# Optimization experiments

Hardware: AMD Instinct MI355X
Metric: run time of the kernel (lower is better)

## Reference

```python
import jax, jax.numpy as jnp
import numpy as np

B = 1024          # batch
S = 2048          # sparseDim == obsDim (required by PhiW shape constraints)
FISTA_ITER = 16


def setup_inputs() -> dict:
    key = jax.random.key(0)
    k1, k2, k3 = jax.random.split(key, 3)
    src = jax.random.normal(k1, (B, S, 1), dtype=jnp.float32)
    Y = jax.random.normal(k2, (B, S, 1), dtype=jnp.float32)
    W = jax.random.normal(k3, (S, S), dtype=jnp.float32)
    # F.normalize(W, p=2, dim=0): unit L2 norm per column
    W = W / jnp.linalg.norm(W, axis=0, keepdims=True)
    alpha = jnp.full((1, 1), 0.1, dtype=jnp.float32)  # alpha_initialize
    return {"src": src, "Y": Y, "W": W, "alpha": alpha}


def reference(src, Y, W, alpha):
    obsDim = W.shape[0]          # == sparseDim == S
    # Lipschitz constant: max |eig(W^T W)|; W^T W is symmetric PSD so eigvalsh is exact
    L = jnp.max(jnp.linalg.eigvalsh(W.T @ W))
    thresh = alpha / L * 0.5     # soft-threshold level, shape [1,1]

    def phiW(x):
        theta_m = x[:, :obsDim]          # [B, S, 1]
        delta = x[:, obsDim:]            # [B, S, 1]
        return src * jnp.matmul(W, theta_m) + delta

    def phiWT(y):
        return jnp.concatenate((jnp.matmul(W.T, src * y), y), axis=1)  # [B, 2S, 1]

    nb = Y.shape[0]
    x0 = jnp.zeros((nb, 2 * obsDim, 1), dtype=Y.dtype)

    def step(carry, _):
        x_old, y_k, t_old = carry
        res = Y - phiW(y_k)
        v = y_k + phiWT(res) / L
        x_new = jnp.sign(v) * jnp.maximum(jnp.abs(v) - thresh, 0.0)
        t_new = (1.0 + jnp.sqrt(1.0 + 4.0 * t_old * t_old)) / 2.0
        y_new = x_new + (t_old - 1.0) / t_new * (x_new - x_old)
        return (x_new, y_new, t_new), None

    (x_new, _, _), _ = jax.lax.scan(
        step, (x0, x0, jnp.float32(1.0)), None, length=FISTA_ITER
    )
    return x_new
```

## Files before the change

### kernel.cpp

```cpp
#include <hip/hip_runtime.h>
#include <math.h>

#define SDIM 2048
#define BATCH 1024
#define NITER 16
#define LM 40

typedef unsigned short ushort_t;
typedef __attribute__((ext_vector_type(8))) short bf16x8;
typedef __attribute__((ext_vector_type(4))) float f32x4;

#define MFMA(a,b,c) __builtin_amdgcn_mfma_f32_16x16x32_bf16((a),(b),(c),0,0,0)

__device__ __forceinline__ float softt(float v, float th){
  return copysignf(fmaxf(fabsf(v) - th, 0.0f), v);
}

__device__ __forceinline__ float bf2f(ushort_t h){
  return __uint_as_float(((unsigned)h) << 16);
}

__device__ __forceinline__ void split2(float x, ushort_t* h, ushort_t* l){
  unsigned u = __float_as_uint(x);
  unsigned hh = (u + 0x7FFFu + ((u >> 16) & 1u)) >> 16;
  float hf = __uint_as_float(hh << 16);
  float r = x - hf;
  unsigned v = __float_as_uint(r);
  unsigned ll = (v + 0x7FFFu + ((v >> 16) & 1u)) >> 16;
  *h = (ushort_t)hh; *l = (ushort_t)ll;
}

__device__ __forceinline__ void cp16(const ushort_t* g, ushort_t* l){
  __builtin_amdgcn_global_load_lds(
      (const __attribute__((address_space(1))) unsigned int*)g,
      (__attribute__((address_space(3))) unsigned int*)l, 16, 0, 0);
}

__device__ __forceinline__ void gemm_core(ushort_t* __restrict__ sm,
                                          const ushort_t* __restrict__ Ah, const ushort_t* __restrict__ Al,
                                          const ushort_t* __restrict__ Bh, const ushort_t* __restrict__ Bl,
                                          int m0, int n0, int K, f32x4 acc[2][2])
{
  ushort_t* lAh = sm;
  ushort_t* lAl = sm + 4096;
  ushort_t* lBh = sm + 8192;
  ushort_t* lBl = sm + 12288;
  const int tid = threadIdx.x;
  const int rr = tid >> 3;
  const int kp = (tid & 7) ^ (rr & 7);
  const size_t strA = (size_t)32 * K;
  const ushort_t* gAh = Ah + (size_t)(m0 + rr) * K + kp * 8;
  const ushort_t* gAl = Al + (size_t)(m0 + rr) * K + kp * 8;
  const ushort_t* gBh = Bh + (size_t)(n0 + rr) * K + kp * 8;
  const ushort_t* gBl = Bl + (size_t)(n0 + rr) * K + kp * 8;
  ushort_t* dA0 = &lAh[tid * 8];      ushort_t* dA1 = &lAh[(tid + 256) * 8];
  ushort_t* dAl0 = &lAl[tid * 8];     ushort_t* dAl1 = &lAl[(tid + 256) * 8];
  ushort_t* dB0 = &lBh[tid * 8];      ushort_t* dB1 = &lBh[(tid + 256) * 8];
  ushort_t* dBl0 = &lBl[tid * 8];     ushort_t* dBl1 = &lBl[(tid + 256) * 8];

  const int lane = tid & 63, wv = tid >> 6;
  const int wm = (wv >> 1) * 32, wn = (wv & 1) * 32;
  const int mm = lane & 15, quad = lane >> 4;
  const int ra0 = wm + mm, ra1 = wm + 16 + mm;
  const int rb0 = wn + mm, rb1 = wn + 16 + mm;
  int oa0[2], oa1[2], ob0[2], ob1[2];
  #pragma unroll
  for (int u = 0; u < 2; u++){
    oa0[u] = ra0*64 + (((u*4 + quad) ^ (ra0 & 7)) << 3);
    oa1[u] = ra1*64 + (((u*4 + quad) ^ (ra1 & 7)) << 3);
    ob0[u] = rb0*64 + (((u*4 + quad) ^ (rb0 & 7)) << 3);
    ob1[u] = rb1*64 + (((u*4 + quad) ^ (rb1 & 7)) << 3);
  }

  const int nk = K / 64;
  cp16(gAh, dA0); cp16(gAh + strA, dA1);
  cp16(gAl, dAl0); cp16(gAl + strA, dAl1);
  cp16(gBh, dB0); cp16(gBh + strA, dB1);
  cp16(gBl, dBl0); cp16(gBl + strA, dBl1);
  gAh += 64; gAl += 64; gBh += 64; gBl += 64;

  for (int kt = 0; kt < nk; kt++){
    __syncthreads();
    bf16x8 ah0[2], ah1[2], al0[2], al1[2], bh0[2], bh1[2], bl0[2], bl1[2];
    #pragma unroll
    for (int u = 0; u < 2; u++){
      ah0[u] = *(const bf16x8*)&lAh[oa0[u]];
      ah1[u] = *(const bf16x8*)&lAh[oa1[u]];
      al0[u] = *(const bf16x8*)&lAl[oa0[u]];
      al1[u] = *(const bf16x8*)&lAl[oa1[u]];
      bh0[u] = *(const bf16x8*)&lBh[ob0[u]];
      bh1[u] = *(const bf16x8*)&lBh[ob1[u]];
      bl0[u] = *(const bf16x8*)&lBl[ob0[u]];
      bl1[u] = *(const bf16x8*)&lBl[ob1[u]];
    }
    __syncthreads();
    if (kt + 1 < nk){
      cp16(gAh, dA0); cp16(gAh + strA, dA1);
      cp16(gAl, dAl0); cp16(gAl + strA, dAl1);
      cp16(gBh, dB0); cp16(gBh + strA, dB1);
      cp16(gBl, dBl0); cp16(gBl + strA, dBl1);
      gAh += 64; gAl += 64; gBh += 64; gBl += 64;
    }
    #pragma unroll
    for (int u = 0; u < 2; u++){
      acc[0][0] = MFMA(ah0[u], bh0[u], acc[0][0]);
      acc[0][0] = MFMA(ah0[u], bl0[u], acc[0][0]);
      acc[0][0] = MFMA(al0[u], bh0[u], acc[0][0]);
      acc[0][1] = MFMA(ah0[u], bh1[u], acc[0][1]);
      acc[0][1] = MFMA(ah0[u], bl1[u], acc[0][1]);
      acc[0][1] = MFMA(al0[u], bh1[u], acc[0][1]);
      acc[1][0] = MFMA(ah1[u], bh0[u], acc[1][0]);
      acc[1][0] = MFMA(ah1[u], bl0[u], acc[1][0]);
      acc[1][0] = MFMA(al1[u], bh0[u], acc[1][0]);
      acc[1][1] = MFMA(ah1[u], bh1[u], acc[1][1]);
      acc[1][1] = MFMA(ah1[u], bl1[u], acc[1][1]);
      acc[1][1] = MFMA(al1[u], bh1[u], acc[1][1]);
    }
  }
}

__device__ __forceinline__ void acc_to_tile(ushort_t* sm, f32x4 acc[2][2]){
  float* tile = (float*)sm;
  const int tid = threadIdx.x, lane = tid & 63, wv = tid >> 6;
  const int wm = (wv >> 1) * 32, wn = (wv & 1) * 32;
  const int mm = lane & 15, quad = lane >> 4;
  #pragma unroll
  for (int tm = 0; tm < 2; tm++)
    #pragma unroll
    for (int tn = 0; tn < 2; tn++)
      #pragma unroll
      for (int i = 0; i < 4; i++)
        tile[(wm + tm*16 + quad*4 + i)*65 + wn + tn*16 + mm] = acc[tm][tn][i];
  __syncthreads();
}

#define EPILOGUE_FOR(rowvar, c4var) \
  const int tid = threadIdx.x, lane = tid & 63, wv = tid >> 6; \
  const int r4 = lane >> 4; \
  const int c4var = (lane & 15) * 4; \
  for (int j = 0; j < 4; j++){ \
    const int rowvar = wv*16 + j*4 + r4;

__global__ __launch_bounds__(256) void k_split(const float* __restrict__ W,
                                               ushort_t* __restrict__ Wah, ushort_t* __restrict__ Wal,
                                               ushort_t* __restrict__ Wbh, ushort_t* __restrict__ Wbl){
  __shared__ float t[32][33];
  const int i0 = blockIdx.y * 32, j0 = blockIdx.x * 32;
  const int r = threadIdx.x >> 3, c = (threadIdx.x & 7) * 4;
  const float4 v = *(const float4*)&W[(size_t)(i0 + r) * SDIM + j0 + c];
  float vv[4] = {v.x, v.y, v.z, v.w};
  ushort_t h[4], l[4];
  #pragma unroll
  for (int q = 0; q < 4; q++){ split2(vv[q], &h[q], &l[q]); t[r][c+q] = vv[q]; }
  *(ushort4*)&Wah[(size_t)(i0 + r) * SDIM + j0 + c] = make_ushort4(h[0],h[1],h[2],h[3]);
  *(ushort4*)&Wal[(size_t)(i0 + r) * SDIM + j0 + c] = make_ushort4(l[0],l[1],l[2],l[3]);
  __syncthreads();
  #pragma unroll
  for (int q = 0; q < 4; q++) split2(t[c+q][r], &h[q], &l[q]);
  *(ushort4*)&Wbh[(size_t)(j0 + r) * SDIM + i0 + c] = make_ushort4(h[0],h[1],h[2],h[3]);
  *(ushort4*)&Wbl[(size_t)(j0 + r) * SDIM + i0 + c] = make_ushort4(l[0],l[1],l[2],l[3]);
}

__global__ __launch_bounds__(256) void k_gemmM(const ushort_t* __restrict__ Wah, const ushort_t* __restrict__ Wal,
                                               float* __restrict__ Mmat){
  __shared__ __align__(16) ushort_t smem[16384];
  const int b = blockIdx.x + (blockIdx.y << 5);
  const int xcd = b & 7, slot = b >> 3;
  const int n0 = (((xcd << 2) + (slot >> 5)) << 6);
  const int m0 = ((slot & 31) << 6);
  f32x4 acc[2][2] = {};
  gemm_core(smem, Wah, Wal, Wah, Wal, m0, n0, SDIM, acc);
  acc_to_tile(smem, acc);
  const float* tile = (const float*)smem;
  EPILOGUE_FOR(row, c4)
    f32x4 a = *(const f32x4*)&tile[row*65 + c4];
    *(f32x4*)&Mmat[(size_t)(m0 + row) * SDIM + n0 + c4] = a;
  }
}

__global__ __launch_bounds__(256) void k_init(float* __restrict__ vRing,
                                              double* __restrict__ dotWV, double* __restrict__ dotWW,
                                              float* __restrict__ betaSq){
  __shared__ float red[256];
  int t = threadIdx.x;
  float vals[8];
  float s = 0.f;
  #pragma unroll
  for (int p = 0; p < 8; p++){
    int j = p*256 + t;
    unsigned h = (unsigned)j * 2654435761u;
    h ^= h >> 16; h *= 2246822519u; h ^= h >> 13;
    float r = (float)(h & 0xFFFFFFu) / 16777216.0f - 0.5f;
    vals[p] = r; s += r*r;
  }
  red[t] = s; __syncthreads();
  for (int o = 128; o > 0; o >>= 1){ if (t < o) red[t] += red[t+o]; __syncthreads(); }
  float inv = rsqrtf(red[0]);
  #pragma unroll
  for (int p = 0; p < 8; p++){
    int j = p*256 + t;
    vRing[SDIM + j] = vals[p]*inv;
    vRing[j] = 0.f;
    vRing[2*SDIM + j] = 0.f;
  }
  if (t < LM+2){ dotWV[t] = 0.0; dotWW[t] = 0.0; betaSq[t] = 0.f; }
}

__global__ __launch_bounds__(256) void k_lstep(const float* __restrict__ M,
    const float* __restrict__ wOld, float* __restrict__ wNew,
    float* __restrict__ vRing, double* __restrict__ dotWV, double* __restrict__ dotWW,
    float* __restrict__ betaSq, int s){
  __shared__ float vs[SDIM];
  __shared__ double pAl[4], pWw[4];
  const int tid = threadIdx.x, bid = blockIdx.x;
  if (s == 1){
    const float* v1 = vRing + SDIM;
    for (int j = tid; j < SDIM; j += 256) vs[j] = v1[j];
  } else {
    const double a  = dotWV[s-1];
    const double ww = dotWW[s-1];
    const float bpSq = betaSq[s-2];
    float bsq = (float)(ww - a*a - (double)bpSq);
    bsq = fmaxf(bsq, 1e-20f);
    const float beta = sqrtf(bsq), invb = 1.0f/beta;
    const float alpha = (float)a, bprev = sqrtf(bpSq);
    const float* vm1 = vRing + ((s-1)%3)*SDIM;
    const float* vm2 = vRing + ((s-2)%3)*SDIM;
    float* vdst = vRing + (s%3)*SDIM;
    for (int j = tid; j < SDIM; j += 256){
      float val = (wOld[j] - alpha*vm1[j] - bprev*vm2[j]) * invb;
      vs[j] = val;
      if (bid == 0) vdst[j] = val;
    }
    if (bid == 0 && tid == 0) betaSq[s-1] = bsq;
  }
  __syncthreads();
  const int wv = tid >> 6, lane = tid & 63;
  const int row = bid*4 + wv;
  const float4* Mr = (const float4*)(M + (size_t)row * SDIM);
  const float4* v4 = (const float4*)vs;
  float acc = 0.f;
  #pragma unroll
  for (int p = 0; p < 8; p++){
    int j4 = p*64 + lane;
    float4 m = Mr[j4], v = v4[j4];
    acc += m.x*v.x + m.y*v.y + m.z*v.z + m.w*v.w;
  }
  #pragma unroll
  for (int o = 32; o > 0; o >>= 1) acc += __shfl_down(acc, o);
  if (lane == 0){
    wNew[row] = acc;
    pAl[wv] = (double)acc * (double)vs[row];
    pWw[wv] = (double)acc * (double)acc;
  }
  __syncthreads();
  if (tid == 0){
    atomicAdd(&dotWV[s], pAl[0]+pAl[1]+pAl[2]+pAl[3]);
    atomicAdd(&dotWW[s], pWw[0]+pWw[1]+pWw[2]+pWw[3]);
  }
}

__global__ void k_sturm(const double* __restrict__ dotWV, const float* __restrict__ betaSq,
                        const float* __restrict__ alphaIn, float* __restrict__ Lbuf){
  __shared__ double sa[LM+1], sb[LM+1];
  int lane = threadIdx.x;
  for (int i = lane; i <= LM; i += 64){
    if (i >= 1){
      sa[i] = dotWV[i];
      sb[i] = (i < LM) ? sqrt((double)betaSq[i]) : 0.0;
    }
  }
  __syncthreads();
  double phi = -1e300, plo = 1e300;
  for (int i = 1 + lane; i <= LM; i += 64){
    double r = (i > 1 ? sb[i-1] : 0.0) + (i < LM ? sb[i] : 0.0);
    phi = fmax(phi, sa[i] + r);
    plo = fmin(plo, sa[i] - r);
  }
  for (int o = 32; o > 0; o >>= 1){
    phi = fmax(phi, __shfl_down(phi, o));
    plo = fmin(plo, __shfl_down(plo, o));
  }
  double hi = __shfl(phi, 0), lo = __shfl(plo, 0);
  for (int round = 0; round < 6; round++){
    double x = lo + (hi - lo) * (double)(lane + 1) / 65.0;
    int cnt = 0;
    double dd = sa[1] - x;
    if (dd < 0) cnt++;
    for (int i = 2; i <= LM; i++){
      double off = sb[i-1];
      if (fabs(dd) < 1e-300) dd = -1e-300;
      dd = sa[i] - x - off*off/dd;
      if (dd < 0) cnt++;
    }
    unsigned long long bal = __ballot(cnt == LM);
    int p = (bal == 0ull) ? 64 : (__ffsll((unsigned long long)bal) - 1);
    double newhi = (p <= 63) ? lo + (hi - lo) * (double)(p + 1) / 65.0 : hi;
    double newlo = (p >= 1)  ? lo + (hi - lo) * (double)p / 65.0       : lo;
    hi = newhi; lo = newlo;
  }
  if (lane == 0){
    double L = 0.5*(lo + hi);
    Lbuf[0] = (float)(1.0 / L);
    Lbuf[1] = (float)(0.5 * (double)alphaIn[0] / L);
  }
}


__global__ __launch_bounds__(256) void k_A0(const float* __restrict__ Y, const float* __restrict__ src,
                                            float* __restrict__ yd, ushort_t* __restrict__ sresh,
                                            ushort_t* __restrict__ sresl, float* __restrict__ out,
                                            const float* __restrict__ Lbuf){
  int idx = blockIdx.x*256 + threadIdx.x;
  float invL = Lbuf[0], th = Lbuf[1];
  float y = Y[idx], s = src[idx];
  split2(s*y, &sresh[idx], &sresl[idx]);
  float xn = softt(y*invL, th);
  int b = idx >> 11, i = idx & 2047;
  out[(size_t)b*4096 + 2048 + i] = xn;
  yd[idx] = xn;
}

__device__ __forceinline__ void swz512(int* m0, int* n0){
  const int b = blockIdx.x + (blockIdx.y << 5);
  const int xcd = b & 7, slot = b >> 3;
  *n0 = (((xcd << 2) + (slot >> 4)) << 6);
  *m0 = ((slot & 15) << 6);
}

__global__ __launch_bounds__(256) void k_gemmA(
    const ushort_t* __restrict__ Wah, const ushort_t* __restrict__ Wal,
    const ushort_t* __restrict__ ymh, const ushort_t* __restrict__ yml,
    const float* __restrict__ Y, const float* __restrict__ src,
    float* __restrict__ yd, float* __restrict__ out,
    ushort_t* __restrict__ sresh, ushort_t* __restrict__ sresl,
    const float* __restrict__ Lbuf, float ck)
{
  __shared__ __align__(16) ushort_t smem[16384];
  f32x4 acc[2][2] = {};
  int m0, n0; swz512(&m0, &n0);
  gemm_core(smem, ymh, yml, Wah, Wal, m0, n0, SDIM, acc);
  acc_to_tile(smem, acc);
  const float* tile = (const float*)smem;
  const float invL = Lbuf[0], th = Lbuf[1];
  EPILOGUE_FOR(row, c4)
    const int brow = m0 + row;
    const size_t g  = (size_t)brow*SDIM + n0 + c4;
    const size_t go = (size_t)brow*4096 + 2048 + n0 + c4;
    f32x4 a   = *(const f32x4*)&tile[row*65 + c4];
    f32x4 s4  = *(const f32x4*)&src[g];
    f32x4 y4  = *(const f32x4*)&Y[g];
    f32x4 yd4 = *(const f32x4*)&yd[g];
    f32x4 xo4 = *(const f32x4*)&out[go];
    f32x4 res, xn, yn;
    ushort4 sh, sl;
    #pragma unroll
    for (int q = 0; q < 4; q++){
      res[q] = y4[q] - s4[q]*a[q] - yd4[q];
      xn[q]  = softt(yd4[q] + res[q]*invL, th);
      yn[q]  = xn[q] + ck*(xn[q] - xo4[q]);
    }
    split2(s4[0]*res[0], &sh.x, &sl.x);
    split2(s4[1]*res[1], &sh.y, &sl.y);
    split2(s4[2]*res[2], &sh.z, &sl.z);
    split2(s4[3]*res[3], &sh.w, &sl.w);
    *(ushort4*)&sresh[g] = sh;
    *(ushort4*)&sresl[g] = sl;
    *(f32x4*)&out[go] = xn;
    *(f32x4*)&yd[g]   = yn;
  }
}

template<bool FIRST>
__global__ __launch_bounds__(256) void k_gemmB(
    const ushort_t* __restrict__ Wbh, const ushort_t* __restrict__ Wbl,
    const ushort_t* __restrict__ sresh, const ushort_t* __restrict__ sresl,
    ushort_t* __restrict__ ymh, ushort_t* __restrict__ yml,
    float* __restrict__ out, const float* __restrict__ Lbuf, float ck)
{
  __shared__ __align__(16) ushort_t smem[16384];
  f32x4 acc[2][2] = {};
  int m0, n0; swz512(&m0, &n0);
  gemm_core(smem, sresh, sresl, Wbh, Wbl, m0, n0, SDIM, acc);
  acc_to_tile(smem, acc);
  const float* tile = (const float*)smem;
  const float invL = Lbuf[0], th = Lbuf[1];
  EPILOGUE_FOR(row, c4)
    const int brow = m0 + row;
    const size_t g  = (size_t)brow*SDIM + n0 + c4;
    const size_t go = (size_t)brow*4096 + n0 + c4;
    f32x4 a = *(const f32x4*)&tile[row*65 + c4];
    f32x4 ym4, xo4;
    if (FIRST){
      ym4 = (f32x4){0.f,0.f,0.f,0.f};
      xo4 = (f32x4){0.f,0.f,0.f,0.f};
    } else {
      ushort4 h4 = *(const ushort4*)&ymh[g];
      ushort4 l4 = *(const ushort4*)&yml[g];
      ym4[0] = bf2f(h4.x) + bf2f(l4.x);
      ym4[1] = bf2f(h4.y) + bf2f(l4.y);
      ym4[2] = bf2f(h4.z) + bf2f(l4.z);
      ym4[3] = bf2f(h4.w) + bf2f(l4.w);
      xo4 = *(const f32x4*)&out[go];
    }
    f32x4 xn, yn;
    ushort4 hh, ll;
    #pragma unroll
    for (int q = 0; q < 4; q++){
      xn[q] = softt(ym4[q] + a[q]*invL, th);
      yn[q] = xn[q] + ck*(xn[q] - xo4[q]);
    }
    split2(yn[0], &hh.x, &ll.x);
    split2(yn[1], &hh.y, &ll.y);
    split2(yn[2], &hh.z, &ll.z);
    split2(yn[3], &hh.w, &ll.w);
    *(f32x4*)&out[go] = xn;
    *(ushort4*)&ymh[g] = hh;
    *(ushort4*)&yml[g] = ll;
  }
}


extern "C" void kernel_launch(void* const* d_in, const int* in_sizes, int n_in,
                              void* d_out, int out_size, void* d_ws, size_t ws_size,
                              hipStream_t stream) {
  const float* src   = (const float*)d_in[0];
  const float* Y     = (const float*)d_in[1];
  const float* W     = (const float*)d_in[2];
  const float* alpha = (const float*)d_in[3];
  float* out = (float*)d_out;
  float* ws  = (float*)d_ws;

  const size_t M1 = 1024*1024;
  float* Mmat = ws;
  float* yd   = ws + 4*M1;
  float* lanc = ws + 6*M1;
  float* w0      = lanc;
  float* w1      = lanc + SDIM;
  float* vRing   = lanc + 2*SDIM;
  double* dotWV  = (double*)(lanc + 5*SDIM);
  double* dotWW  = dotWV + 128;
  float* betaSq  = lanc + 5*SDIM + 512;
  float* Lbuf    = betaSq + 128;
  ushort_t* u16 = (ushort_t*)(ws + 7*M1);
  ushort_t* Wah = u16;
  ushort_t* Wal = u16 + 4*M1;
  ushort_t* Wbh = u16 + 8*M1;
  ushort_t* Wbl = u16 + 12*M1;
  ushort_t* ymh = u16 + 16*M1;
  ushort_t* yml = u16 + 18*M1;
  ushort_t* sresh = u16 + 20*M1;
  ushort_t* sresl = u16 + 22*M1;

  k_split<<<dim3(64,64), 256, 0, stream>>>(W, Wah, Wal, Wbh, Wbl);
  k_gemmM<<<dim3(32,32), 256, 0, stream>>>(Wah, Wal, Mmat);

  float* wb[2] = { w0, w1 };
  k_init<<<1, 256, 0, stream>>>(vRing, dotWV, dotWW, betaSq);
  for (int s = 1; s <= LM; s++){
    k_lstep<<<512, 256, 0, stream>>>(Mmat, wb[(s+1)&1], wb[s&1], vRing, dotWV, dotWW, betaSq, s);
  }
  k_sturm<<<1, 64, 0, stream>>>(dotWV, betaSq, alpha, Lbuf);

  double t = 1.0;
  float ckv[NITER];
  for (int k = 0; k < NITER; k++){
    double tn = 0.5*(1.0 + sqrt(1.0 + 4.0*t*t));
    ckv[k] = (float)((t - 1.0)/tn);
    t = tn;
  }

  k_A0<<<(BATCH*SDIM)/256, 256, 0, stream>>>(Y, src, yd, sresh, sresl, out, Lbuf);
  k_gemmB<true><<<dim3(32,16), 256, 0, stream>>>(Wbh, Wbl, sresh, sresl, ymh, yml, out, Lbuf, ckv[0]);
  for (int k = 1; k < NITER; k++){
    k_gemmA<<<dim3(32,16), 256, 0, stream>>>(Wah, Wal, ymh, yml, Y, src, yd, out, sresh, sresl, Lbuf, ckv[k]);
    k_gemmB<false><<<dim3(32,16), 256, 0, stream>>>(Wbh, Wbl, sresh, sresl, ymh, yml, out, Lbuf, ckv[k]);
  }
  (void)in_sizes; (void)n_in; (void)out_size; (void)ws_size;
}
```

Measured before the change: 1.708 ms.

## Pre-pack W into MFMA fragment layout and load B operand directly to registers

The split kernel now writes the bf16 hi/lo copies of W and W^T in a 16x32 fragment-tiled layout that matches the MFMA operand layout. The GEMM core then reads the W operand straight from global memory into registers, double-buffered one k-step ahead, instead of staging it through LDS. Only the activation operand still goes through LDS, which halves LDS usage and the LDS read traffic per step. The trade-off is that W tiles are no longer shared through LDS across waves, so each wave issues its own global loads, and there is more register pressure from the prefetched fragments.

```diff
diff --git a/kernel.cpp b/kernel.cpp
--- a/kernel.cpp
+++ b/kernel.cpp
@@ -36,87 +36,128 @@
       (__attribute__((address_space(3))) unsigned int*)l, 16, 0, 0);
 }
 
-__device__ __forceinline__ void gemm_core(ushort_t* __restrict__ sm,
-                                          const ushort_t* __restrict__ Ah, const ushort_t* __restrict__ Al,
-                                          const ushort_t* __restrict__ Bh, const ushort_t* __restrict__ Bl,
-                                          int m0, int n0, int K, f32x4 acc[2][2])
+template<bool AFRAG>
+__device__ __forceinline__ void gemm_core3(ushort_t* __restrict__ sm,
+    const ushort_t* __restrict__ Ah, const ushort_t* __restrict__ Al,
+    const ushort_t* __restrict__ Bfh, const ushort_t* __restrict__ Bfl,
+    int m0, int n0, int K, f32x4 acc[2][2])
 {
-  ushort_t* lAh = sm;
-  ushort_t* lAl = sm + 4096;
-  ushort_t* lBh = sm + 8192;
-  ushort_t* lBl = sm + 12288;
   const int tid = threadIdx.x;
-  const int rr = tid >> 3;
-  const int kp = (tid & 7) ^ (rr & 7);
-  const size_t strA = (size_t)32 * K;
-  const ushort_t* gAh = Ah + (size_t)(m0 + rr) * K + kp * 8;
-  const ushort_t* gAl = Al + (size_t)(m0 + rr) * K + kp * 8;
-  const ushort_t* gBh = Bh + (size_t)(n0 + rr) * K + kp * 8;
-  const ushort_t* gBl = Bl + (size_t)(n0 + rr) * K + kp * 8;
-  ushort_t* dA0 = &lAh[tid * 8];      ushort_t* dA1 = &lAh[(tid + 256) * 8];
-  ushort_t* dAl0 = &lAl[tid * 8];     ushort_t* dAl1 = &lAl[(tid + 256) * 8];
-  ushort_t* dB0 = &lBh[tid * 8];      ushort_t* dB1 = &lBh[(tid + 256) * 8];
-  ushort_t* dBl0 = &lBl[tid * 8];     ushort_t* dBl1 = &lBl[(tid + 256) * 8];
-
   const int lane = tid & 63, wv = tid >> 6;
-  const int wm = (wv >> 1) * 32, wn = (wv & 1) * 32;
+  const int wm = (wv >> 1) * 32;
   const int mm = lane & 15, quad = lane >> 4;
-  const int ra0 = wm + mm, ra1 = wm + 16 + mm;
-  const int rb0 = wn + mm, rb1 = wn + 16 + mm;
-  int oa0[2], oa1[2], ob0[2], ob1[2];
-  #pragma unroll
-  for (int u = 0; u < 2; u++){
-    oa0[u] = ra0*64 + (((u*4 + quad) ^ (ra0 & 7)) << 3);
-    oa1[u] = ra1*64 + (((u*4 + quad) ^ (ra1 & 7)) << 3);
-    ob0[u] = rb0*64 + (((u*4 + quad) ^ (rb0 & 7)) << 3);
-    ob1[u] = rb1*64 + (((u*4 + quad) ^ (rb1 & 7)) << 3);
-  }
-
-  const int nk = K / 64;
-  cp16(gAh, dA0); cp16(gAh + strA, dA1);
-  cp16(gAl, dAl0); cp16(gAl + strA, dAl1);
-  cp16(gBh, dB0); cp16(gBh + strA, dB1);
-  cp16(gBl, dBl0); cp16(gBl + strA, dBl1);
-  gAh += 64; gAl += 64; gBh += 64; gBl += 64;
-
-  for (int kt = 0; kt < nk; kt++){
-    __syncthreads();
-    bf16x8 ah0[2], ah1[2], al0[2], al1[2], bh0[2], bh1[2], bl0[2], bl1[2];
+  const int KS = K >> 5;
+
+  const ushort_t *gA0, *gA1, *gA2, *gA3;
+  int astep;
+  if (!AFRAG){
+    const int rr = tid >> 3;
+    const int kp = (tid & 7) ^ (rr & 7);
+    gA0 = Ah + (size_t)(m0 + rr) * K + kp * 8;
+    gA1 = Ah + (size_t)(m0 + rr + 32) * K + kp * 8;
+    gA2 = Al + (size_t)(m0 + rr) * K + kp * 8;
+    gA3 = Al + (size_t)(m0 + rr + 32) * K + kp * 8;
+    astep = 64;
+  } else {
+    const int nt0 = m0 >> 4;
+    const int id0 = tid, id1 = tid + 256;
+    gA0 = Ah + ((size_t)(nt0 + (id0 >> 7)) * KS + ((id0 >> 6) & 1)) * 512 + (id0 & 63) * 8;
+    gA1 = Ah + ((size_t)(nt0 + (id1 >> 7)) * KS + ((id1 >> 6) & 1)) * 512 + (id1 & 63) * 8;
+    gA2 = Al + ((size_t)(nt0 + (id0 >> 7)) * KS + ((id0 >> 6) & 1)) * 512 + (id0 & 63) * 8;
+    gA3 = Al + ((size_t)(nt0 + (id1 >> 7)) * KS + ((id1 >> 6) & 1)) * 512 + (id1 & 63) * 8;
+    astep = 1024;
+  }
+  ushort_t* dA0 = &sm[tid * 8];
+  ushort_t* dA1 = &sm[(tid + 256) * 8];
+  ushort_t* dA2 = &sm[4096 + tid * 8];
+  ushort_t* dA3 = &sm[4096 + (tid + 256) * 8];
+
+  int oa[2][2];
+  if (!AFRAG){
+    #pragma unroll
+    for (int s = 0; s < 2; s++){
+      const int ra = wm + s*16 + mm;
+      #pragma unroll
+      for (int u = 0; u < 2; u++)
+        oa[s][u] = ra*64 + (((u*4 + quad) ^ (ra & 7)) << 3);
+    }
+  } else {
+    #pragma unroll
+    for (int s = 0; s < 2; s++){
+      const int ntl = (wv >> 1)*2 + s;
+      #pragma unroll
+      for (int u = 0; u < 2; u++)
+        oa[s][u] = (ntl*2 + u)*512 + lane*8;
+    }
+  }
+
+  const ushort_t* pBh[2]; const ushort_t* pBl[2];
+  #pragma unroll
+  for (int s = 0; s < 2; s++){
+    const int nt = (n0 >> 4) + (wv & 1)*2 + s;
+    pBh[s] = Bfh + (size_t)nt * KS * 512 + lane*8;
+    pBl[s] = Bfl + (size_t)nt * KS * 512 + lane*8;
+  }
+
+  const int nk = K >> 6;
+  cp16(gA0, dA0); cp16(gA1, dA1); cp16(gA2, dA2); cp16(gA3, dA3);
+  bf16x8 bhP[2][2], blP[2][2], bhQ[2][2], blQ[2][2];
+  #pragma unroll
+  for (int s = 0; s < 2; s++)
     #pragma unroll
     for (int u = 0; u < 2; u++){
-      ah0[u] = *(const bf16x8*)&lAh[oa0[u]];
-      ah1[u] = *(const bf16x8*)&lAh[oa1[u]];
-      al0[u] = *(const bf16x8*)&lAl[oa0[u]];
-      al1[u] = *(const bf16x8*)&lAl[oa1[u]];
-      bh0[u] = *(const bf16x8*)&lBh[ob0[u]];
-      bh1[u] = *(const bf16x8*)&lBh[ob1[u]];
-      bl0[u] = *(const bf16x8*)&lBl[ob0[u]];
-      bl1[u] = *(const bf16x8*)&lBl[ob1[u]];
-    }
-    __syncthreads();
-    if (kt + 1 < nk){
-      cp16(gAh, dA0); cp16(gAh + strA, dA1);
-      cp16(gAl, dAl0); cp16(gAl + strA, dAl1);
-      cp16(gBh, dB0); cp16(gBh + strA, dB1);
-      cp16(gBl, dBl0); cp16(gBl + strA, dBl1);
-      gAh += 64; gAl += 64; gBh += 64; gBl += 64;
-    }
-    #pragma unroll
-    for (int u = 0; u < 2; u++){
-      acc[0][0] = MFMA(ah0[u], bh0[u], acc[0][0]);
-      acc[0][0] = MFMA(ah0[u], bl0[u], acc[0][0]);
-      acc[0][0] = MFMA(al0[u], bh0[u], acc[0][0]);
-      acc[0][1] = MFMA(ah0[u], bh1[u], acc[0][1]);
-      acc[0][1] = MFMA(ah0[u], bl1[u], acc[0][1]);
-      acc[0][1] = MFMA(al0[u], bh1[u], acc[0][1]);
-      acc[1][0] = MFMA(ah1[u], bh0[u], acc[1][0]);
-      acc[1][0] = MFMA(ah1[u], bl0[u], acc[1][0]);
-      acc[1][0] = MFMA(al1[u], bh0[u], acc[1][0]);
-      acc[1][1] = MFMA(ah1[u], bh1[u], acc[1][1]);
-      acc[1][1] = MFMA(ah1[u], bl1[u], acc[1][1]);
-      acc[1][1] = MFMA(al1[u], bh1[u], acc[1][1]);
-    }
-  }
+      bhP[s][u] = *(const bf16x8*)(pBh[s] + (size_t)u*512);
+      blP[s][u] = *(const bf16x8*)(pBl[s] + (size_t)u*512);
+    }
+
+#define GK_STEP(KT, BH, BL, BHN, BLN, PF) { \
+    __syncthreads();   \
+    bf16x8 ah[2][2], al8[2][2]; \
+    _Pragma("unroll") \
+    for (int s = 0; s < 2; s++){ \
+      _Pragma("unroll") \
+      for (int u = 0; u < 2; u++){ \
+        ah[s][u]  = *(const bf16x8*)&sm[oa[s][u]]; \
+        al8[s][u] = *(const bf16x8*)&sm[4096 + oa[s][u]]; \
+      } \
+    } \
+    __syncthreads();   \
+    if (PF){ \
+      const size_t ao = (size_t)(KT + 1) * astep; \
+      cp16(gA0 + ao, dA0); cp16(gA1 + ao, dA1); \
+      cp16(gA2 + ao, dA2); cp16(gA3 + ao, dA3); \
+      const size_t bo = (size_t)(KT + 1) * 1024; \
+      _Pragma("unroll") \
+      for (int s = 0; s < 2; s++){ \
+        _Pragma("unroll") \
+        for (int u = 0; u < 2; u++){ \
+          BHN[s][u] = *(const bf16x8*)(pBh[s] + bo + u*512); \
+          BLN[s][u] = *(const bf16x8*)(pBl[s] + bo + u*512); \
+        } \
+      } \
+    } \
+    _Pragma("unroll") \
+    for (int u = 0; u < 2; u++){ \
+      acc[0][0] = MFMA(ah[0][u],  BH[0][u], acc[0][0]); \
+      acc[0][0] = MFMA(ah[0][u],  BL[0][u], acc[0][0]); \
+      acc[0][0] = MFMA(al8[0][u], BH[0][u], acc[0][0]); \
+      acc[0][1] = MFMA(ah[0][u],  BH[1][u], acc[0][1]); \
+      acc[0][1] = MFMA(ah[0][u],  BL[1][u], acc[0][1]); \
+      acc[0][1] = MFMA(al8[0][u], BH[1][u], acc[0][1]); \
+      acc[1][0] = MFMA(ah[1][u],  BH[0][u], acc[1][0]); \
+      acc[1][0] = MFMA(ah[1][u],  BL[0][u], acc[1][0]); \
+      acc[1][0] = MFMA(al8[1][u], BH[0][u], acc[1][0]); \
+      acc[1][1] = MFMA(ah[1][u],  BH[1][u], acc[1][1]); \
+      acc[1][1] = MFMA(ah[1][u],  BL[1][u], acc[1][1]); \
+      acc[1][1] = MFMA(al8[1][u], BH[1][u], acc[1][1]); \
+    } \
+  }
+
+  for (int kt = 0; kt < nk; kt += 2){
+    GK_STEP(kt,     bhP, blP, bhQ, blQ, true);
+    GK_STEP(kt + 1, bhQ, blQ, bhP, blP, (kt + 2 < nk));
+  }
+#undef GK_STEP
 }
 
 __device__ __forceinline__ void acc_to_tile(ushort_t* sm, f32x4 acc[2][2]){
@@ -142,8 +183,8 @@
     const int rowvar = wv*16 + j*4 + r4;
 
 __global__ __launch_bounds__(256) void k_split(const float* __restrict__ W,
-                                               ushort_t* __restrict__ Wah, ushort_t* __restrict__ Wal,
-                                               ushort_t* __restrict__ Wbh, ushort_t* __restrict__ Wbl){
+        ushort_t* __restrict__ Wfa_h, ushort_t* __restrict__ Wfa_l,
+        ushort_t* __restrict__ Wfb_h, ushort_t* __restrict__ Wfb_l){
   __shared__ float t[32][33];
   const int i0 = blockIdx.y * 32, j0 = blockIdx.x * 32;
   const int r = threadIdx.x >> 3, c = (threadIdx.x & 7) * 4;
@@ -152,24 +193,35 @@
   ushort_t h[4], l[4];
   #pragma unroll
   for (int q = 0; q < 4; q++){ split2(vv[q], &h[q], &l[q]); t[r][c+q] = vv[q]; }
-  *(ushort4*)&Wah[(size_t)(i0 + r) * SDIM + j0 + c] = make_ushort4(h[0],h[1],h[2],h[3]);
-  *(ushort4*)&Wal[(size_t)(i0 + r) * SDIM + j0 + c] = make_ushort4(l[0],l[1],l[2],l[3]);
+  {
+    const int row = i0 + r, col = j0 + c;
+    const size_t idx = ((size_t)(row >> 4) * 64 + (col >> 5)) * 512
+                     + (size_t)((col >> 3) & 3) * 128 + (row & 15) * 8 + (col & 7);
+    *(ushort4*)&Wfa_h[idx] = make_ushort4(h[0],h[1],h[2],h[3]);
+    *(ushort4*)&Wfa_l[idx] = make_ushort4(l[0],l[1],l[2],l[3]);
+  }
   __syncthreads();
   #pragma unroll
   for (int q = 0; q < 4; q++) split2(t[c+q][r], &h[q], &l[q]);
-  *(ushort4*)&Wbh[(size_t)(j0 + r) * SDIM + i0 + c] = make_ushort4(h[0],h[1],h[2],h[3]);
-  *(ushort4*)&Wbl[(size_t)(j0 + r) * SDIM + i0 + c] = make_ushort4(l[0],l[1],l[2],l[3]);
-}
-
-__global__ __launch_bounds__(256) void k_gemmM(const ushort_t* __restrict__ Wah, const ushort_t* __restrict__ Wal,
+  {
+    const int row = j0 + r, col = i0 + c;
+    const size_t idx = ((size_t)(row >> 4) * 64 + (col >> 5)) * 512
+                     + (size_t)((col >> 3) & 3) * 128 + (row & 15) * 8 + (col & 7);
+    *(ushort4*)&Wfb_h[idx] = make_ushort4(h[0],h[1],h[2],h[3]);
+    *(ushort4*)&Wfb_l[idx] = make_ushort4(l[0],l[1],l[2],l[3]);
+  }
+}
+
+__global__ __launch_bounds__(256) void k_gemmM(const ushort_t* __restrict__ Wfa_h,
+                                               const ushort_t* __restrict__ Wfa_l,
                                                float* __restrict__ Mmat){
-  __shared__ __align__(16) ushort_t smem[16384];
+  __shared__ __align__(16) ushort_t smem[8320];
   const int b = blockIdx.x + (blockIdx.y << 5);
   const int xcd = b & 7, slot = b >> 3;
   const int n0 = (((xcd << 2) + (slot >> 5)) << 6);
   const int m0 = ((slot & 31) << 6);
   f32x4 acc[2][2] = {};
-  gemm_core(smem, Wah, Wal, Wah, Wal, m0, n0, SDIM, acc);
+  gemm_core3<true>(smem, Wfa_h, Wfa_l, Wfa_h, Wfa_l, m0, n0, SDIM, acc);
   acc_to_tile(smem, acc);
   const float* tile = (const float*)smem;
   EPILOGUE_FOR(row, c4)
@@ -329,17 +381,17 @@
 }
 
 __global__ __launch_bounds__(256) void k_gemmA(
-    const ushort_t* __restrict__ Wah, const ushort_t* __restrict__ Wal,
+    const ushort_t* __restrict__ Wfa_h, const ushort_t* __restrict__ Wfa_l,
     const ushort_t* __restrict__ ymh, const ushort_t* __restrict__ yml,
     const float* __restrict__ Y, const float* __restrict__ src,
     float* __restrict__ yd, float* __restrict__ out,
     ushort_t* __restrict__ sresh, ushort_t* __restrict__ sresl,
     const float* __restrict__ Lbuf, float ck)
 {
-  __shared__ __align__(16) ushort_t smem[16384];
+  __shared__ __align__(16) ushort_t smem[8320];
   f32x4 acc[2][2] = {};
   int m0, n0; swz512(&m0, &n0);
-  gemm_core(smem, ymh, yml, Wah, Wal, m0, n0, SDIM, acc);
+  gemm_core3<false>(smem, ymh, yml, Wfa_h, Wfa_l, m0, n0, SDIM, acc);
   acc_to_tile(smem, acc);
   const float* tile = (const float*)smem;
   const float invL = Lbuf[0], th = Lbuf[1];
@@ -373,15 +425,15 @@
 
 template<bool FIRST>
 __global__ __launch_bounds__(256) void k_gemmB(
-    const ushort_t* __restrict__ Wbh, const ushort_t* __restrict__ Wbl,
+    const ushort_t* __restrict__ Wfb_h, const ushort_t* __restrict__ Wfb_l,
     const ushort_t* __restrict__ sresh, const ushort_t* __restrict__ sresl,
     ushort_t* __restrict__ ymh, ushort_t* __restrict__ yml,
     float* __restrict__ out, const float* __restrict__ Lbuf, float ck)
 {
-  __shared__ __align__(16) ushort_t smem[16384];
+  __shared__ __align__(16) ushort_t smem[8320];
   f32x4 acc[2][2] = {};
   int m0, n0; swz512(&m0, &n0);
-  gemm_core(smem, sresh, sresl, Wbh, Wbl, m0, n0, SDIM, acc);
+  gemm_core3<false>(smem, sresh, sresl, Wfb_h, Wfb_l, m0, n0, SDIM, acc);
   acc_to_tile(smem, acc);
   const float* tile = (const float*)smem;
   const float invL = Lbuf[0], th = Lbuf[1];
@@ -443,17 +495,17 @@
   float* betaSq  = lanc + 5*SDIM + 512;
   float* Lbuf    = betaSq + 128;
   ushort_t* u16 = (ushort_t*)(ws + 7*M1);
-  ushort_t* Wah = u16;
-  ushort_t* Wal = u16 + 4*M1;
-  ushort_t* Wbh = u16 + 8*M1;
-  ushort_t* Wbl = u16 + 12*M1;
+  ushort_t* Wfa_h = u16;
+  ushort_t* Wfa_l = u16 + 4*M1;
+  ushort_t* Wfb_h = u16 + 8*M1;
+  ushort_t* Wfb_l = u16 + 12*M1;
   ushort_t* ymh = u16 + 16*M1;
   ushort_t* yml = u16 + 18*M1;
   ushort_t* sresh = u16 + 20*M1;
   ushort_t* sresl = u16 + 22*M1;
 
-  k_split<<<dim3(64,64), 256, 0, stream>>>(W, Wah, Wal, Wbh, Wbl);
-  k_gemmM<<<dim3(32,32), 256, 0, stream>>>(Wah, Wal, Mmat);
+  k_split<<<dim3(64,64), 256, 0, stream>>>(W, Wfa_h, Wfa_l, Wfb_h, Wfb_l);
+  k_gemmM<<<dim3(32,32), 256, 0, stream>>>(Wfa_h, Wfa_l, Mmat);
 
   float* wb[2] = { w0, w1 };
   k_init<<<1, 256, 0, stream>>>(vRing, dotWV, dotWW, betaSq);
@@ -471,10 +523,10 @@
   }
 
   k_A0<<<(BATCH*SDIM)/256, 256, 0, stream>>>(Y, src, yd, sresh, sresl, out, Lbuf);
-  k_gemmB<true><<<dim3(32,16), 256, 0, stream>>>(Wbh, Wbl, sresh, sresl, ymh, yml, out, Lbuf, ckv[0]);
+  k_gemmB<true><<<dim3(32,16), 256, 0, stream>>>(Wfb_h, Wfb_l, sresh, sresl, ymh, yml, out, Lbuf, ckv[0]);
   for (int k = 1; k < NITER; k++){
-    k_gemmA<<<dim3(32,16), 256, 0, stream>>>(Wah, Wal, ymh, yml, Y, src, yd, out, sresh, sresl, Lbuf, ckv[k]);
-    k_gemmB<false><<<dim3(32,16), 256, 0, stream>>>(Wbh, Wbl, sresh, sresl, ymh, yml, out, Lbuf, ckv[k]);
+    k_gemmA<<<dim3(32,16), 256, 0, stream>>>(Wfa_h, Wfa_l, ymh, yml, Y, src, yd, out, sresh, sresl, Lbuf, ckv[k]);
+    k_gemmB<false><<<dim3(32,16), 256, 0, stream>>>(Wfb_h, Wfb_l, sresh, sresl, ymh, yml, out, Lbuf, ckv[k]);
   }
   (void)in_sizes; (void)n_in; (void)out_size; (void)ws_size;
 }
```

Measured after the change: 1.969 ms. 1.15x slower.

## Use triple-buffered K=32 LDS pipeline with vmcnt waits in GEMM core

Applied to the files above, without the earlier changes.

Replaces the single-buffer K=64 GEMM mainloop with a three-stage ring of K=32 tiles. Global-to-LDS loads run two stages ahead, and each iteration uses one s_waitcnt vmcnt plus a barrier instead of two __syncthreads. MFMA issue is wrapped in s_setprio to favour the math waves. This is meant to hide global load latency and cut barrier stalls, at the cost of more LDS per block (48KB), which could lower occupancy, and more loop iterations.

```diff
diff --git a/kernel.cpp b/kernel.cpp
--- a/kernel.cpp
+++ b/kernel.cpp
@@ -36,90 +36,79 @@
       (__attribute__((address_space(3))) unsigned int*)l, 16, 0, 0);
 }
 
-__device__ __forceinline__ void gemm_core(ushort_t* __restrict__ sm,
-                                          const ushort_t* __restrict__ Ah, const ushort_t* __restrict__ Al,
-                                          const ushort_t* __restrict__ Bh, const ushort_t* __restrict__ Bl,
-                                          int m0, int n0, int K, f32x4 acc[2][2])
+__device__ __forceinline__ void gemm_core5(ushort_t* __restrict__ sm,
+    const ushort_t* __restrict__ Ah, const ushort_t* __restrict__ Al,
+    const ushort_t* __restrict__ Bh, const ushort_t* __restrict__ Bl,
+    int m0, int n0, int K, f32x4 acc[2][2])
 {
-  ushort_t* lAh = sm;
-  ushort_t* lAl = sm + 4096;
-  ushort_t* lBh = sm + 8192;
-  ushort_t* lBl = sm + 12288;
   const int tid = threadIdx.x;
-  const int rr = tid >> 3;
-  const int kp = (tid & 7) ^ (rr & 7);
-  const size_t strA = (size_t)32 * K;
+  const int rr = tid >> 2;
+  const int kc = tid & 3;
+  const int kp = kc ^ (rr & 3);
   const ushort_t* gAh = Ah + (size_t)(m0 + rr) * K + kp * 8;
   const ushort_t* gAl = Al + (size_t)(m0 + rr) * K + kp * 8;
   const ushort_t* gBh = Bh + (size_t)(n0 + rr) * K + kp * 8;
   const ushort_t* gBl = Bl + (size_t)(n0 + rr) * K + kp * 8;
-  ushort_t* dA0 = &lAh[tid * 8];      ushort_t* dA1 = &lAh[(tid + 256) * 8];
-  ushort_t* dAl0 = &lAl[tid * 8];     ushort_t* dAl1 = &lAl[(tid + 256) * 8];
-  ushort_t* dB0 = &lBh[tid * 8];      ushort_t* dB1 = &lBh[(tid + 256) * 8];
-  ushort_t* dBl0 = &lBl[tid * 8];     ushort_t* dBl1 = &lBl[(tid + 256) * 8];
 
   const int lane = tid & 63, wv = tid >> 6;
   const int wm = (wv >> 1) * 32, wn = (wv & 1) * 32;
   const int mm = lane & 15, quad = lane >> 4;
-  const int ra0 = wm + mm, ra1 = wm + 16 + mm;
-  const int rb0 = wn + mm, rb1 = wn + 16 + mm;
-  int oa0[2], oa1[2], ob0[2], ob1[2];
-  #pragma unroll
-  for (int u = 0; u < 2; u++){
-    oa0[u] = ra0*64 + (((u*4 + quad) ^ (ra0 & 7)) << 3);
-    oa1[u] = ra1*64 + (((u*4 + quad) ^ (ra1 & 7)) << 3);
-    ob0[u] = rb0*64 + (((u*4 + quad) ^ (rb0 & 7)) << 3);
-    ob1[u] = rb1*64 + (((u*4 + quad) ^ (rb1 & 7)) << 3);
-  }
-
-  const int nk = K / 64;
-  cp16(gAh, dA0); cp16(gAh + strA, dA1);
-  cp16(gAl, dAl0); cp16(gAl + strA, dAl1);
-  cp16(gBh, dB0); cp16(gBh + strA, dB1);
-  cp16(gBl, dBl0); cp16(gBl + strA, dBl1);
-  gAh += 64; gAl += 64; gBh += 64; gBl += 64;
-
-  for (int kt = 0; kt < nk; kt++){
-    __syncthreads();
-    bf16x8 ah0[2], ah1[2], al0[2], al1[2], bh0[2], bh1[2], bl0[2], bl1[2];
+  int oa[2], ob[2];
+  #pragma unroll
+  for (int s = 0; s < 2; s++){
+    const int ra = wm + s*16 + mm;
+    const int rb = wn + s*16 + mm;
+    oa[s] = ra*32 + ((quad ^ (ra & 3)) << 3);
+    ob[s] = rb*32 + ((quad ^ (rb & 3)) << 3);
+  }
+
+  const int NT = K >> 5;
+
+#define STAGE5(T) { \
+    ushort_t* b_ = sm + ((T) % 3) * 8192; \
+    const size_t o_ = (size_t)(T) * 32; \
+    cp16(gAh + o_, b_ + tid*8); \
+    cp16(gAl + o_, b_ + 2048 + tid*8); \
+    cp16(gBh + o_, b_ + 4096 + tid*8); \
+    cp16(gBl + o_, b_ + 6144 + tid*8); \
+  }
+
+  STAGE5(0);
+  STAGE5(1);
+
+  for (int kt = 0; kt < NT; kt++){
+    if (kt + 1 < NT) asm volatile("s_waitcnt vmcnt(4)\ns_barrier" ::: "memory");
+    else             asm volatile("s_waitcnt vmcnt(0)\ns_barrier" ::: "memory");
+    if (kt + 2 < NT) STAGE5(kt + 2);
+    const ushort_t* b = sm + (kt % 3) * 8192;
+    bf16x8 ah[2], al8[2], bh[2], bl8[2];
     #pragma unroll
-    for (int u = 0; u < 2; u++){
-      ah0[u] = *(const bf16x8*)&lAh[oa0[u]];
-      ah1[u] = *(const bf16x8*)&lAh[oa1[u]];
-      al0[u] = *(const bf16x8*)&lAl[oa0[u]];
-      al1[u] = *(const bf16x8*)&lAl[oa1[u]];
-      bh0[u] = *(const bf16x8*)&lBh[ob0[u]];
-      bh1[u] = *(const bf16x8*)&lBh[ob1[u]];
-      bl0[u] = *(const bf16x8*)&lBl[ob0[u]];
-      bl1[u] = *(const bf16x8*)&lBl[ob1[u]];
-    }
-    __syncthreads();
-    if (kt + 1 < nk){
-      cp16(gAh, dA0); cp16(gAh + strA, dA1);
-      cp16(gAl, dAl0); cp16(gAl + strA, dAl1);
-      cp16(gBh, dB0); cp16(gBh + strA, dB1);
-      cp16(gBl, dBl0); cp16(gBl + strA, dBl1);
-      gAh += 64; gAl += 64; gBh += 64; gBl += 64;
-    }
-    #pragma unroll
-    for (int u = 0; u < 2; u++){
-      acc[0][0] = MFMA(ah0[u], bh0[u], acc[0][0]);
-      acc[0][0] = MFMA(ah0[u], bl0[u], acc[0][0]);
-      acc[0][0] = MFMA(al0[u], bh0[u], acc[0][0]);
-      acc[0][1] = MFMA(ah0[u], bh1[u], acc[0][1]);
-      acc[0][1] = MFMA(ah0[u], bl1[u], acc[0][1]);
-      acc[0][1] = MFMA(al0[u], bh1[u], acc[0][1]);
-      acc[1][0] = MFMA(ah1[u], bh0[u], acc[1][0]);
-      acc[1][0] = MFMA(ah1[u], bl0[u], acc[1][0]);
-      acc[1][0] = MFMA(al1[u], bh0[u], acc[1][0]);
-      acc[1][1] = MFMA(ah1[u], bh1[u], acc[1][1]);
-      acc[1][1] = MFMA(ah1[u], bl1[u], acc[1][1]);
-      acc[1][1] = MFMA(al1[u], bh1[u], acc[1][1]);
-    }
-  }
+    for (int s = 0; s < 2; s++){
+      ah[s]  = *(const bf16x8*)&b[oa[s]];
+      al8[s] = *(const bf16x8*)&b[2048 + oa[s]];
+      bh[s]  = *(const bf16x8*)&b[4096 + ob[s]];
+      bl8[s] = *(const bf16x8*)&b[6144 + ob[s]];
+    }
+    __builtin_amdgcn_s_setprio(1);
+    acc[0][0] = MFMA(ah[0],  bh[0],  acc[0][0]);
+    acc[0][0] = MFMA(ah[0],  bl8[0], acc[0][0]);
+    acc[0][0] = MFMA(al8[0], bh[0],  acc[0][0]);
+    acc[0][1] = MFMA(ah[0],  bh[1],  acc[0][1]);
+    acc[0][1] = MFMA(ah[0],  bl8[1], acc[0][1]);
+    acc[0][1] = MFMA(al8[0], bh[1],  acc[0][1]);
+    acc[1][0] = MFMA(ah[1],  bh[0],  acc[1][0]);
+    acc[1][0] = MFMA(ah[1],  bl8[0], acc[1][0]);
+    acc[1][0] = MFMA(al8[1], bh[0],  acc[1][0]);
+    acc[1][1] = MFMA(ah[1],  bh[1],  acc[1][1]);
+    acc[1][1] = MFMA(ah[1],  bl8[1], acc[1][1]);
+    acc[1][1] = MFMA(al8[1], bh[1],  acc[1][1]);
+    __builtin_amdgcn_s_setprio(0);
+  }
+#undef STAGE5
 }
 
 __device__ __forceinline__ void acc_to_tile(ushort_t* sm, f32x4 acc[2][2]){
+  __syncthreads();
   float* tile = (float*)sm;
   const int tid = threadIdx.x, lane = tid & 63, wv = tid >> 6;
   const int wm = (wv >> 1) * 32, wn = (wv & 1) * 32;
@@ -163,13 +152,13 @@
 
 __global__ __launch_bounds__(256) void k_gemmM(const ushort_t* __restrict__ Wah, const ushort_t* __restrict__ Wal,
                                                float* __restrict__ Mmat){
-  __shared__ __align__(16) ushort_t smem[16384];
+  __shared__ __align__(16) ushort_t smem[24576];
   const int b = blockIdx.x + (blockIdx.y << 5);
   const int xcd = b & 7, slot = b >> 3;
   const int n0 = (((xcd << 2) + (slot >> 5)) << 6);
   const int m0 = ((slot & 31) << 6);
   f32x4 acc[2][2] = {};
-  gemm_core(smem, Wah, Wal, Wah, Wal, m0, n0, SDIM, acc);
+  gemm_core5(smem, Wah, Wal, Wah, Wal, m0, n0, SDIM, acc);
   acc_to_tile(smem, acc);
   const float* tile = (const float*)smem;
   EPILOGUE_FOR(row, c4)
@@ -336,10 +325,10 @@
     ushort_t* __restrict__ sresh, ushort_t* __restrict__ sresl,
     const float* __restrict__ Lbuf, float ck)
 {
-  __shared__ __align__(16) ushort_t smem[16384];
+  __shared__ __align__(16) ushort_t smem[24576];
   f32x4 acc[2][2] = {};
   int m0, n0; swz512(&m0, &n0);
-  gemm_core(smem, ymh, yml, Wah, Wal, m0, n0, SDIM, acc);
+  gemm_core5(smem, ymh, yml, Wah, Wal, m0, n0, SDIM, acc);
   acc_to_tile(smem, acc);
   const float* tile = (const float*)smem;
   const float invL = Lbuf[0], th = Lbuf[1];
@@ -378,10 +367,10 @@
     ushort_t* __restrict__ ymh, ushort_t* __restrict__ yml,
     float* __restrict__ out, const float* __restrict__ Lbuf, float ck)
 {
-  __shared__ __align__(16) ushort_t smem[16384];
+  __shared__ __align__(16) ushort_t smem[24576];
   f32x4 acc[2][2] = {};
   int m0, n0; swz512(&m0, &n0);
-  gemm_core(smem, sresh, sresl, Wbh, Wbl, m0, n0, SDIM, acc);
+  gemm_core5(smem, sresh, sresl, Wbh, Wbl, m0, n0, SDIM, acc);
   acc_to_tile(smem, acc);
   const float* tile = (const float*)smem;
   const float invL = Lbuf[0], th = Lbuf[1];
```

Result: slower. 1.963 ms (+14.9%).

## Double-buffer LDS staging in batch GEMMs and reorder block tile mapping

Applied to the files above, without the earlier changes.

Adds a double-buffered GEMM core for the two per-iteration batch GEMMs. The next K-tile's global-to-LDS copy is issued into the alternate buffer right after a single barrier, which drops one barrier per K step and lets the copy overlap the MFMA work. The block-to-tile swizzle for all GEMMs also changes so consecutive slots walk across N within an XCD before moving along M, which changes L2 reuse. In exchange LDS per block doubles to 64KB, which may lower occupancy.

```diff
diff --git a/kernel.cpp b/kernel.cpp
--- a/kernel.cpp
+++ b/kernel.cpp
@@ -41,6 +41,7 @@
                                           const ushort_t* __restrict__ Bh, const ushort_t* __restrict__ Bl,
                                           int m0, int n0, int K, f32x4 acc[2][2])
 {
+  constexpr int BK = 64;
   ushort_t* lAh = sm;
   ushort_t* lAl = sm + 4096;
   ushort_t* lBh = sm + 8192;
@@ -53,10 +54,6 @@
   const ushort_t* gAl = Al + (size_t)(m0 + rr) * K + kp * 8;
   const ushort_t* gBh = Bh + (size_t)(n0 + rr) * K + kp * 8;
   const ushort_t* gBl = Bl + (size_t)(n0 + rr) * K + kp * 8;
-  ushort_t* dA0 = &lAh[tid * 8];      ushort_t* dA1 = &lAh[(tid + 256) * 8];
-  ushort_t* dAl0 = &lAl[tid * 8];     ushort_t* dAl1 = &lAl[(tid + 256) * 8];
-  ushort_t* dB0 = &lBh[tid * 8];      ushort_t* dB1 = &lBh[(tid + 256) * 8];
-  ushort_t* dBl0 = &lBl[tid * 8];     ushort_t* dBl1 = &lBl[(tid + 256) * 8];
 
   const int lane = tid & 63, wv = tid >> 6;
   const int wm = (wv >> 1) * 32, wn = (wv & 1) * 32;
@@ -66,18 +63,18 @@
   int oa0[2], oa1[2], ob0[2], ob1[2];
   #pragma unroll
   for (int u = 0; u < 2; u++){
-    oa0[u] = ra0*64 + (((u*4 + quad) ^ (ra0 & 7)) << 3);
-    oa1[u] = ra1*64 + (((u*4 + quad) ^ (ra1 & 7)) << 3);
-    ob0[u] = rb0*64 + (((u*4 + quad) ^ (rb0 & 7)) << 3);
-    ob1[u] = rb1*64 + (((u*4 + quad) ^ (rb1 & 7)) << 3);
-  }
-
-  const int nk = K / 64;
-  cp16(gAh, dA0); cp16(gAh + strA, dA1);
-  cp16(gAl, dAl0); cp16(gAl + strA, dAl1);
-  cp16(gBh, dB0); cp16(gBh + strA, dB1);
-  cp16(gBl, dBl0); cp16(gBl + strA, dBl1);
-  gAh += 64; gAl += 64; gBh += 64; gBl += 64;
+    oa0[u] = ra0*BK + (((u*4 + quad) ^ (ra0 & 7)) << 3);
+    oa1[u] = ra1*BK + (((u*4 + quad) ^ (ra1 & 7)) << 3);
+    ob0[u] = rb0*BK + (((u*4 + quad) ^ (rb0 & 7)) << 3);
+    ob1[u] = rb1*BK + (((u*4 + quad) ^ (rb1 & 7)) << 3);
+  }
+
+  const int nk = K / BK;
+  cp16(gAh, &lAh[tid*8]); cp16(gAh + strA, &lAh[(tid+256)*8]);
+  cp16(gAl, &lAl[tid*8]); cp16(gAl + strA, &lAl[(tid+256)*8]);
+  cp16(gBh, &lBh[tid*8]); cp16(gBh + strA, &lBh[(tid+256)*8]);
+  cp16(gBl, &lBl[tid*8]); cp16(gBl + strA, &lBl[(tid+256)*8]);
+  gAh += BK; gAl += BK; gBh += BK; gBl += BK;
 
   for (int kt = 0; kt < nk; kt++){
     __syncthreads();
@@ -95,11 +92,11 @@
     }
     __syncthreads();
     if (kt + 1 < nk){
-      cp16(gAh, dA0); cp16(gAh + strA, dA1);
-      cp16(gAl, dAl0); cp16(gAl + strA, dAl1);
-      cp16(gBh, dB0); cp16(gBh + strA, dB1);
-      cp16(gBl, dBl0); cp16(gBl + strA, dBl1);
-      gAh += 64; gAl += 64; gBh += 64; gBl += 64;
+      cp16(gAh, &lAh[tid*8]); cp16(gAh + strA, &lAh[(tid+256)*8]);
+      cp16(gAl, &lAl[tid*8]); cp16(gAl + strA, &lAl[(tid+256)*8]);
+      cp16(gBh, &lBh[tid*8]); cp16(gBh + strA, &lBh[(tid+256)*8]);
+      cp16(gBl, &lBl[tid*8]); cp16(gBl + strA, &lBl[(tid+256)*8]);
+      gAh += BK; gAl += BK; gBh += BK; gBl += BK;
     }
     #pragma unroll
     for (int u = 0; u < 2; u++){
@@ -119,6 +116,85 @@
   }
 }
 
+__device__ __forceinline__ void gemm_coreF(ushort_t* __restrict__ sm,
+    const ushort_t* __restrict__ Ah, const ushort_t* __restrict__ Al,
+    const ushort_t* __restrict__ Bh, const ushort_t* __restrict__ Bl,
+    int m0, int n0, int K, f32x4 acc[2][2])
+{
+  constexpr int BK = 64;
+  const int tid = threadIdx.x;
+  const int rr = tid >> 3;
+  const int kp = (tid & 7) ^ (rr & 7);
+  const size_t strA = (size_t)32 * K;
+  const ushort_t* gAh = Ah + (size_t)(m0 + rr) * K + kp * 8;
+  const ushort_t* gAl = Al + (size_t)(m0 + rr) * K + kp * 8;
+  const ushort_t* gBh = Bh + (size_t)(n0 + rr) * K + kp * 8;
+  const ushort_t* gBl = Bl + (size_t)(n0 + rr) * K + kp * 8;
+
+  const int lane = tid & 63, wv = tid >> 6;
+  const int wm = (wv >> 1) * 32, wn = (wv & 1) * 32;
+  const int mm = lane & 15, quad = lane >> 4;
+  const int ra0 = wm + mm, ra1 = wm + 16 + mm;
+  const int rb0 = wn + mm, rb1 = wn + 16 + mm;
+  int oa0[2], oa1[2], ob0[2], ob1[2];
+  #pragma unroll
+  for (int u = 0; u < 2; u++){
+    oa0[u] = ra0*BK + (((u*4 + quad) ^ (ra0 & 7)) << 3);
+    oa1[u] = ra1*BK + (((u*4 + quad) ^ (ra1 & 7)) << 3);
+    ob0[u] = rb0*BK + (((u*4 + quad) ^ (rb0 & 7)) << 3);
+    ob1[u] = rb1*BK + (((u*4 + quad) ^ (rb1 & 7)) << 3);
+  }
+
+  const int nk = K / BK;
+
+#define STAGEF(T) { \
+    ushort_t* d_ = sm + (((T) & 1) << 14); \
+    const size_t o_ = (size_t)(T) * BK; \
+    cp16(gAh + o_, &d_[tid*8]);          cp16(gAh + o_ + strA, &d_[(tid+256)*8]); \
+    cp16(gAl + o_, &d_[4096 + tid*8]);   cp16(gAl + o_ + strA, &d_[4096 + (tid+256)*8]); \
+    cp16(gBh + o_, &d_[8192 + tid*8]);   cp16(gBh + o_ + strA, &d_[8192 + (tid+256)*8]); \
+    cp16(gBl + o_, &d_[12288 + tid*8]);  cp16(gBl + o_ + strA, &d_[12288 + (tid+256)*8]); \
+  }
+
+  STAGEF(0);
+  for (int kt = 0; kt < nk; kt++){
+    __syncthreads();
+    if (kt + 1 < nk) STAGEF(kt + 1);
+    const ushort_t* lAh = sm + ((kt & 1) << 14);
+    const ushort_t* lAl = lAh + 4096;
+    const ushort_t* lBh = lAh + 8192;
+    const ushort_t* lBl = lAh + 12288;
+    bf16x8 ah0[2], ah1[2], al0[2], al1[2], bh0[2], bh1[2], bl0[2], bl1[2];
+    #pragma unroll
+    for (int u = 0; u < 2; u++){
+      ah0[u] = *(const bf16x8*)&lAh[oa0[u]];
+      ah1[u] = *(const bf16x8*)&lAh[oa1[u]];
+      al0[u] = *(const bf16x8*)&lAl[oa0[u]];
+      al1[u] = *(const bf16x8*)&lAl[oa1[u]];
+      bh0[u] = *(const bf16x8*)&lBh[ob0[u]];
+      bh1[u] = *(const bf16x8*)&lBh[ob1[u]];
+      bl0[u] = *(const bf16x8*)&lBl[ob0[u]];
+      bl1[u] = *(const bf16x8*)&lBl[ob1[u]];
+    }
+    #pragma unroll
+    for (int u = 0; u < 2; u++){
+      acc[0][0] = MFMA(ah0[u], bh0[u], acc[0][0]);
+      acc[0][0] = MFMA(ah0[u], bl0[u], acc[0][0]);
+      acc[0][0] = MFMA(al0[u], bh0[u], acc[0][0]);
+      acc[0][1] = MFMA(ah0[u], bh1[u], acc[0][1]);
+      acc[0][1] = MFMA(ah0[u], bl1[u], acc[0][1]);
+      acc[0][1] = MFMA(al0[u], bh1[u], acc[0][1]);
+      acc[1][0] = MFMA(ah1[u], bh0[u], acc[1][0]);
+      acc[1][0] = MFMA(ah1[u], bl0[u], acc[1][0]);
+      acc[1][0] = MFMA(al1[u], bh0[u], acc[1][0]);
+      acc[1][1] = MFMA(ah1[u], bh1[u], acc[1][1]);
+      acc[1][1] = MFMA(ah1[u], bl1[u], acc[1][1]);
+      acc[1][1] = MFMA(al1[u], bh1[u], acc[1][1]);
+    }
+  }
+#undef STAGEF
+}
+
 __device__ __forceinline__ void acc_to_tile(ushort_t* sm, f32x4 acc[2][2]){
   float* tile = (float*)sm;
   const int tid = threadIdx.x, lane = tid & 63, wv = tid >> 6;
@@ -166,8 +242,8 @@
   __shared__ __align__(16) ushort_t smem[16384];
   const int b = blockIdx.x + (blockIdx.y << 5);
   const int xcd = b & 7, slot = b >> 3;
-  const int n0 = (((xcd << 2) + (slot >> 5)) << 6);
-  const int m0 = ((slot & 31) << 6);
+  const int n0 = (((xcd << 2) + (slot & 3)) << 6);
+  const int m0 = ((slot >> 2) << 6);
   f32x4 acc[2][2] = {};
   gemm_core(smem, Wah, Wal, Wah, Wal, m0, n0, SDIM, acc);
   acc_to_tile(smem, acc);
@@ -324,8 +400,8 @@
 __device__ __forceinline__ void swz512(int* m0, int* n0){
   const int b = blockIdx.x + (blockIdx.y << 5);
   const int xcd = b & 7, slot = b >> 3;
-  *n0 = (((xcd << 2) + (slot >> 4)) << 6);
-  *m0 = ((slot & 15) << 6);
+  *n0 = (((xcd << 2) + (slot & 3)) << 6);
+  *m0 = ((slot >> 2) << 6);
 }
 
 __global__ __launch_bounds__(256) void k_gemmA(
@@ -336,10 +412,10 @@
     ushort_t* __restrict__ sresh, ushort_t* __restrict__ sresl,
     const float* __restrict__ Lbuf, float ck)
 {
-  __shared__ __align__(16) ushort_t smem[16384];
+  __shared__ __align__(16) ushort_t smem[32768];
   f32x4 acc[2][2] = {};
   int m0, n0; swz512(&m0, &n0);
-  gemm_core(smem, ymh, yml, Wah, Wal, m0, n0, SDIM, acc);
+  gemm_coreF(smem, ymh, yml, Wah, Wal, m0, n0, SDIM, acc);
   acc_to_tile(smem, acc);
   const float* tile = (const float*)smem;
   const float invL = Lbuf[0], th = Lbuf[1];
@@ -378,10 +454,10 @@
     ushort_t* __restrict__ ymh, ushort_t* __restrict__ yml,
     float* __restrict__ out, const float* __restrict__ Lbuf, float ck)
 {
-  __shared__ __align__(16) ushort_t smem[16384];
+  __shared__ __align__(16) ushort_t smem[32768];
   f32x4 acc[2][2] = {};
   int m0, n0; swz512(&m0, &n0);
-  gemm_core(smem, sresh, sresl, Wbh, Wbl, m0, n0, SDIM, acc);
+  gemm_coreF(smem, sresh, sresl, Wbh, Wbl, m0, n0, SDIM, acc);
   acc_to_tile(smem, acc);
   const float* tile = (const float*)smem;
   const float invL = Lbuf[0], th = Lbuf[1];
```

Measured after the change: 1.680 ms, median of 2. Within noise of the previous version (-1.7%).
